# Optimization experiments

Measured on AMD Instinct MI355X. Metric: run time of the kernel, lower is better.

Reference implementation:

```python
import jax, jax.numpy as jnp
import numpy as np

D, H, WIN, OUT = 3, 64, 8, 32
B, T = 128, 129
IU, JU = np.triu_indices(D, k=1)  # Lyndon pairs i<j at depth 2


def setup_inputs() -> dict:
    key = jax.random.key(0)
    ks = jax.random.split(key, 10)
    ts = jnp.broadcast_to(jnp.linspace(0.0, 1.0, T), (B, T))
    # path-like control values: cumulative sum of small increments
    x = jnp.cumsum(0.1 * jax.random.normal(ks[0], (B, T, D)), axis=1)
    def lin(k, o, i):
        return jax.random.normal(k, (o, i), dtype=jnp.float32) * (1.0 / np.sqrt(i))
    return {
        "ts": ts, "x": x,
        "W0": lin(ks[1], 128, D), "b0": jnp.zeros((128,), jnp.float32),
        "W1": lin(ks[2], 128, 128), "b1": jnp.zeros((128,), jnp.float32),
        "W2": lin(ks[3], H, 128), "b2": jnp.zeros((H,), jnp.float32),
        "V0": lin(ks[4], 128, H), "c0": jnp.zeros((128,), jnp.float32),
        "V1": lin(ks[5], 128, 128), "c1": jnp.zeros((128,), jnp.float32),
        "V2": lin(ks[6], D * H, 128), "c2": jnp.zeros((D * H,), jnp.float32),
        "R": lin(ks[7], OUT, H), "rb": jnp.zeros((OUT,), jnp.float32),
    }


def reference(ts, x, W0, b0, W1, b1, W2, b2, V0, c0, V1, c1, V2, c2, R, rb):
    sp = jax.nn.softplus

    def init_mlp(v):  # R^D -> R^H, Euclidean retract = identity
        return W2 @ sp(W1 @ sp(W0 @ v + b0) + b1) + b2

    def vf_flat(y):  # R^H -> R^{D*H}, final tanh (split_multi_vector_field)
        return jnp.tanh(V2 @ sp(V1 @ sp(V0 @ y + c0) + c1) + c2)

    def F(y):
        # level-1 fields f_i(y) as rows of m: (D, H)
        m = vf_flat(y).reshape(D, H)
        # J[a, b] = D f_b(y) . f_a(y)  via JVPs in directions f_a
        J = jax.vmap(lambda v: jax.jvp(vf_flat, (y,), (v,))[1].reshape(D, H))(m)
        # Lyndon level-2 brackets [f_i, f_j] = Df_j.f_i - Df_i.f_j
        br = J[IU, JU] - J[JU, IU]  # (D*(D-1)/2, H)
        return jnp.concatenate([m, br], axis=0).T  # (H, logsig_size)

    def logsigs_fn(xs):  # depth-2 log-signatures over disjoint windows
        nw = (T - 1) // WIN
        idx = (np.arange(nw) * WIN)[:, None] + np.arange(WIN + 1)[None, :]
        win = xs[idx]
        lvl1 = win[:, -1] - win[:, 0]       # increments
        rel = win[:, :-1] - win[:, :1]      # path relative to window start
        dv = win[:, 1:] - win[:, :-1]       # increments within window
        a = jnp.einsum('nki,nkj->nij', rel, dv)
        area = 0.5 * (a - jnp.swapaxes(a, 1, 2))  # Levy areas
        return jnp.concatenate([lvl1, area[:, IU, JU]], axis=1)

    def solve_one(t, xs):
        h0 = init_mlp(xs[0])
        ls = logsigs_fn(xs)                       # (nw, L)
        t_sig = t[::WIN]                          # window knot times
        slopes = ls / (t_sig[1:] - t_sig[:-1])[:, None]  # dz/dt per window
        slope_steps = jnp.repeat(slopes, WIN, axis=0)    # (T-1, L)
        dts = t[1:] - t[:-1]

        def step(y, inp):  # Heun integration of dy = F(y) dz/dt dt
            dt, s = inp
            k1 = F(y) @ s
            k2 = F(y + dt * k1) @ s
            yn = y + 0.5 * dt * (k1 + k2)
            return yn, yn

        _, ys = jax.lax.scan(step, h0, (dts, slope_steps))
        hidden = jnp.concatenate([h0[None], ys], axis=0)  # (T, H)
        return jnp.tanh(hidden @ R.T + rb)                # evolving readout

    return jax.vmap(solve_one)(ts, x)  # (B, T, OUT)
```

## Files before the change

### kernel.cpp

```cpp
#include <hip/hip_runtime.h>
#include <math.h>

#define BB 128
#define TT 129
#define NSTEP 128
#define NW 16
#define WINW 8
#define OUTD 32

typedef _Float16 h2_t __attribute__((ext_vector_type(2)));

__device__ __forceinline__ float fast_rcp(float v){ return __builtin_amdgcn_rcpf(v); }
__device__ __forceinline__ float softplus_f(float v){ return fmaxf(v,0.f)+__logf(1.f+__expf(-fabsf(v))); }
__device__ __forceinline__ float sigmoid_f(float v){ return fast_rcp(1.f+__expf(-v)); }
__device__ __forceinline__ float tanh_f(float v){
    float ax=fminf(fabsf(v),15.f); float e=__expf(2.f*ax);
    float r=1.f-2.f*fast_rcp(e+1.f); return copysignf(r,v);
}
__device__ __forceinline__ float pack2(float a,float b){
    h2_t h; h.x=(_Float16)a; h.y=(_Float16)b; return __builtin_bit_cast(float,h);
}
__device__ __forceinline__ float dot2c(float wc,float ac,float acc){
    return __builtin_amdgcn_fdot2(__builtin_bit_cast(h2_t,wc),__builtin_bit_cast(h2_t,ac),acc,false);
}
__device__ __forceinline__ float dot2q(float4 wq,float4 aq,float acc){
    acc=dot2c(wq.x,aq.x,acc); acc=dot2c(wq.y,aq.y,acc);
    acc=dot2c(wq.z,aq.z,acc); acc=dot2c(wq.w,aq.w,acc); return acc;
}
#define DOT4(acc,Wv,Av) acc += (Wv).x*(Av).x + (Wv).y*(Av).y + (Wv).z*(Av).z + (Wv).w*(Av).w
#define PIN4(v) asm volatile("" : "+v"((v).x), "+v"((v).y), "+v"((v).z), "+v"((v).w))

#define DPPF(x,ctrl) __builtin_bit_cast(float, __builtin_amdgcn_update_dpp(0, __builtin_bit_cast(int,(x)), (ctrl), 0xF, 0xF, true))
__device__ __forceinline__ float dpp_xor1(float x){ return DPPF(x,0xB1); }
__device__ __forceinline__ float dpp_xor2(float x){ return DPPF(x,0x4E); }
__device__ __forceinline__ float dpp_hmir(float x){ return DPPF(x,0x141); }
#define RED8(x) do{ x += dpp_xor1(x); x += dpp_xor2(x); x += dpp_hmir(x); }while(0)

__global__ __launch_bounds__(512, 1)
void ncde_solve(const float* __restrict__ ts, const float* __restrict__ x,
                const float* __restrict__ W0, const float* __restrict__ b0,
                const float* __restrict__ W1, const float* __restrict__ b1,
                const float* __restrict__ W2, const float* __restrict__ b2,
                const float* __restrict__ V0, const float* __restrict__ c0,
                const float* __restrict__ V1, const float* __restrict__ c1,
                const float* __restrict__ V2, const float* __restrict__ c2,
                const float* __restrict__ R, const float* __restrict__ rb,
                float* __restrict__ out)
{
    const int b = blockIdx.x;
    const int t = threadIdx.x;
    const int r = t >> 3, q = t & 7;
    const int prow = t >> 3, poct = t & 7;

    __shared__ __align__(16) float RSh[OUTD*68];
    __shared__ __align__(16) float ySh[64];
    __shared__ __align__(16) float yp[32], y2p[32];
    __shared__ __align__(16) float a0H[64], a1H[64];
    __shared__ __align__(16) float mpH[96];
    __shared__ __align__(16) float u0H[192], u1H[192];
    __shared__ float slopesSh[NW][6];
    __shared__ float dtsSh[NSTEP];

    float4 v0c[2], v1c[2][2], v2c[3][2];
    {
        auto pkld = [](const float* src)->float4{
            const float4* p=(const float4*)src;
            float4 a=p[0], c=p[1];
            float4 rr; rr.x=pack2(a.x,a.y); rr.y=pack2(a.z,a.w); rr.z=pack2(c.x,c.y); rr.w=pack2(c.z,c.w);
            return rr;
        };
        #pragma unroll
        for (int i=0;i<2;i++) v0c[i]=pkld(V0 + (r+64*i)*64 + q*8);
        #pragma unroll
        for (int i=0;i<2;i++){
            const float* base = V1 + (r+64*i)*128 + q*16;
            v1c[i][0]=pkld(base); v1c[i][1]=pkld(base+8);
        }
        #pragma unroll
        for (int i=0;i<3;i++){
            const float* base = V2 + (r+64*i)*128 + q*16;
            v2c[i][0]=pkld(base); v2c[i][1]=pkld(base+8);
        }
        #pragma unroll
        for (int i=0;i<2;i++) PIN4(v0c[i]);
        #pragma unroll
        for (int i=0;i<2;i++){ PIN4(v1c[i][0]); PIN4(v1c[i][1]); }
        #pragma unroll
        for (int i=0;i<3;i++){ PIN4(v2c[i][0]); PIN4(v2c[i][1]); }
    }
    const float c0A=c0[r], c0B=c0[64+r];
    const float c1A=c1[r], c1B=c1[64+r];
    const float c2A=c2[r], c2B=c2[64+r], c2C=c2[128+r];
    const float rbp = rb[prow & 31];

    for (int i=t; i<OUTD*64; i+=512) RSh[(i>>6)*68 + (i&63)] = R[i];
    const float* tsb = ts + (size_t)b*TT;
    if (t < NSTEP) dtsSh[t] = tsb[t+1] - tsb[t];

    if (t < NW) {
        const int w = t;
        const float* xs = x + (size_t)(b*TT + w*WINW)*3;
        float x0c[3] = {xs[0], xs[1], xs[2]};
        float prev[3] = {x0c[0], x0c[1], x0c[2]};
        float am01=0.f, am02=0.f, am12=0.f, am10=0.f, am20=0.f, am21=0.f;
        #pragma unroll
        for (int k=0;k<WINW;k++) {
            float cur[3] = {xs[(k+1)*3+0], xs[(k+1)*3+1], xs[(k+1)*3+2]};
            float rel[3], dv[3];
            #pragma unroll
            for (int c=0;c<3;c++){ rel[c]=prev[c]-x0c[c]; dv[c]=cur[c]-prev[c]; }
            am01 += rel[0]*dv[1]; am10 += rel[1]*dv[0];
            am02 += rel[0]*dv[2]; am20 += rel[2]*dv[0];
            am12 += rel[1]*dv[2]; am21 += rel[2]*dv[1];
            prev[0]=cur[0]; prev[1]=cur[1]; prev[2]=cur[2];
        }
        const float invden = 1.f/(tsb[(w+1)*WINW] - tsb[w*WINW]);
        slopesSh[w][0] = (prev[0]-x0c[0])*invden;
        slopesSh[w][1] = (prev[1]-x0c[1])*invden;
        slopesSh[w][2] = (prev[2]-x0c[2])*invden;
        slopesSh[w][3] = 0.5f*(am01-am10)*invden;
        slopesSh[w][4] = 0.5f*(am02-am20)*invden;
        slopesSh[w][5] = 0.5f*(am12-am21)*invden;
    }

    if (t < 128) {
        const float xv0 = x[(size_t)b*TT*3+0];
        const float xv1 = x[(size_t)b*TT*3+1];
        const float xv2 = x[(size_t)b*TT*3+2];
        float acc = b0[t] + W0[t*3]*xv0 + W0[t*3+1]*xv1 + W0[t*3+2]*xv2;
        u0H[t] = softplus_f(acc);
    }
    __syncthreads();
    if (t < 128) {
        float acc = b1[t];
        const float4* rw = (const float4*)(W1 + t*128);
        #pragma unroll 8
        for (int k=0;k<32;k++){ float4 wv=rw[k]; float4 av=*(const float4*)&u0H[4*k]; DOT4(acc,wv,av); }
        u1H[t] = softplus_f(acc);
    }
    __syncthreads();
    if (t < 64) {
        float acc = b2[t];
        const float4* rw = (const float4*)(W2 + t*128);
        #pragma unroll 8
        for (int k=0;k<32;k++){ float4 wv=rw[k]; float4 av=*(const float4*)&u1H[4*k]; DOT4(acc,wv,av); }
        ySh[t] = acc;
        ((_Float16*)yp)[t] = (_Float16)acc;
    }
    __syncthreads();

    float yreg = ySh[r];
    float k1r = 0.f;
    float S0,S1,S2,S3,S4,S5;

    auto Feval = [&](const float* ypIn, bool first, float dtc) {
        float sig0A,sig0B,sig1A,sig1B,mA,mB,mC,dtA,dtB,dtC;
        {
            float4 y0 = ((const float4*)ypIn)[q];
            float zA=dot2q(v0c[0],y0,0.f);
            float zB=dot2q(v0c[1],y0,0.f);
            RED8(zA); RED8(zB);
            zA += c0A; zB += c0B;
            sig0A=sigmoid_f(zA); sig0B=sigmoid_f(zB);
            if (!q){
                ((_Float16*)a0H)[r]    = (_Float16)softplus_f(zA);
                ((_Float16*)a0H)[64+r] = (_Float16)softplus_f(zB);
            }
        }
        __syncthreads();
        {
            const float4* A = (const float4*)a0H + q*2;
            float4 a0=A[0], a1=A[1];
            float zA=dot2q(v1c[0][0],a0,0.f); zA=dot2q(v1c[0][1],a1,zA);
            float zB=dot2q(v1c[1][0],a0,0.f); zB=dot2q(v1c[1][1],a1,zB);
            RED8(zA); RED8(zB);
            zA += c1A; zB += c1B;
            sig1A=sigmoid_f(zA); sig1B=sigmoid_f(zB);
            if (!q){
                ((_Float16*)a1H)[r]    = (_Float16)softplus_f(zA);
                ((_Float16*)a1H)[64+r] = (_Float16)softplus_f(zB);
            }
        }
        __syncthreads();
        {
            const float4* A = (const float4*)a1H + q*2;
            float4 a0=A[0], a1=A[1];
            float zA=dot2q(v2c[0][0],a0,0.f); zA=dot2q(v2c[0][1],a1,zA);
            float zB=dot2q(v2c[1][0],a0,0.f); zB=dot2q(v2c[1][1],a1,zB);
            float zC=dot2q(v2c[2][0],a0,0.f); zC=dot2q(v2c[2][1],a1,zC);
            RED8(zA); RED8(zB); RED8(zC);
            mA=tanh_f(zA+c2A); mB=tanh_f(zB+c2B); mC=tanh_f(zC+c2C);
            dtA=1.f-mA*mA; dtB=1.f-mB*mB; dtC=1.f-mC*mC;
            if (!q){
                ((_Float16*)mpH)[r]     = (_Float16)mA;
                ((_Float16*)mpH)[64+r]  = (_Float16)mB;
                ((_Float16*)mpH)[128+r] = (_Float16)mC;
            }
        }
        __syncthreads();
        {
            const float4* M = (const float4*)mpH;
            float4 g0=M[q], g1=M[8+q], g2=M[16+q];
            float t0A=dot2q(v0c[0],g0,0.f), t1A=dot2q(v0c[0],g1,0.f), t2A=dot2q(v0c[0],g2,0.f);
            float t0B=dot2q(v0c[1],g0,0.f), t1B=dot2q(v0c[1],g1,0.f), t2B=dot2q(v0c[1],g2,0.f);
            RED8(t0A); RED8(t1A); RED8(t2A);
            RED8(t0B); RED8(t1B); RED8(t2B);
            if (!q){
                ((_Float16*)u0H)[r]      = (_Float16)(sig0A*t0A);
                ((_Float16*)u0H)[64+r]   = (_Float16)(sig0B*t0B);
                ((_Float16*)u0H)[128+r]  = (_Float16)(sig0A*t1A);
                ((_Float16*)u0H)[192+r]  = (_Float16)(sig0B*t1B);
                ((_Float16*)u0H)[256+r]  = (_Float16)(sig0A*t2A);
                ((_Float16*)u0H)[320+r]  = (_Float16)(sig0B*t2B);
            }
        }
        __syncthreads();
        {
            const float4* U = (const float4*)u0H;
            float4 g0a=U[q*2],    g0b=U[q*2+1];
            float4 g1a=U[16+q*2], g1b=U[16+q*2+1];
            float4 g2a=U[32+q*2], g2b=U[32+q*2+1];
            float t0A=dot2q(v1c[0][0],g0a,0.f); t0A=dot2q(v1c[0][1],g0b,t0A);
            float t1A=dot2q(v1c[0][0],g1a,0.f); t1A=dot2q(v1c[0][1],g1b,t1A);
            float t2A=dot2q(v1c[0][0],g2a,0.f); t2A=dot2q(v1c[0][1],g2b,t2A);
            float t0B=dot2q(v1c[1][0],g0a,0.f); t0B=dot2q(v1c[1][1],g0b,t0B);
            float t1B=dot2q(v1c[1][0],g1a,0.f); t1B=dot2q(v1c[1][1],g1b,t1B);
            float t2B=dot2q(v1c[1][0],g2a,0.f); t2B=dot2q(v1c[1][1],g2b,t2B);
            RED8(t0A); RED8(t1A); RED8(t2A);
            RED8(t0B); RED8(t1B); RED8(t2B);
            if (!q){
                ((_Float16*)u1H)[r]      = (_Float16)(sig1A*t0A);
                ((_Float16*)u1H)[64+r]   = (_Float16)(sig1B*t0B);
                ((_Float16*)u1H)[128+r]  = (_Float16)(sig1A*t1A);
                ((_Float16*)u1H)[192+r]  = (_Float16)(sig1B*t1B);
                ((_Float16*)u1H)[256+r]  = (_Float16)(sig1A*t2A);
                ((_Float16*)u1H)[320+r]  = (_Float16)(sig1B*t2B);
            }
        }
        __syncthreads();
        {
            const float4* U = (const float4*)u1H;
            float4 g0a=U[q*2],    g0b=U[q*2+1];
            float4 g1a=U[16+q*2], g1b=U[16+q*2+1];
            float4 g2a=U[32+q*2], g2b=U[32+q*2+1];
            float J1r=dot2q(v2c[0][0],g1a,0.f); J1r=dot2q(v2c[0][1],g1b,J1r);
            float J2r=dot2q(v2c[0][0],g2a,0.f); J2r=dot2q(v2c[0][1],g2b,J2r);
            float J0m=dot2q(v2c[1][0],g0a,0.f); J0m=dot2q(v2c[1][1],g0b,J0m);
            float J2m=dot2q(v2c[1][0],g2a,0.f); J2m=dot2q(v2c[1][1],g2b,J2m);
            float J0t=dot2q(v2c[2][0],g0a,0.f); J0t=dot2q(v2c[2][1],g0b,J0t);
            float J1t=dot2q(v2c[2][0],g1a,0.f); J1t=dot2q(v2c[2][1],g1b,J1t);
            RED8(J1r); RED8(J2r); RED8(J0m); RED8(J2m); RED8(J0t); RED8(J1t);
            J1r*=dtA; J2r*=dtA; J0m*=dtB; J2m*=dtB; J0t*=dtC; J1t*=dtC;
            float kk = mA*S0 + mB*S1 + mC*S2
                     + S3*(J0m - J1r) + S4*(J0t - J2r) + S5*(J1t - J2m);
            if (first){
                k1r = kk;
                float y2 = yreg + dtc*kk;
                if (!q) ((_Float16*)y2p)[r] = (_Float16)y2;
            } else {
                yreg += 0.5f*dtc*(k1r + kk);
                if (!q){ ((_Float16*)yp)[r] = (_Float16)yreg; ySh[r] = yreg; }
            }
        }
        __syncthreads();
    };

    auto proj = [&](int stp) {
        if (t < 256){
            const float4* rr = (const float4*)(RSh + prow*68 + poct*8);
            const float4* yy = (const float4*)(ySh + poct*8);
            float pacc = 0.f;
            DOT4(pacc, rr[0], yy[0]); DOT4(pacc, rr[1], yy[1]);
            pacc += dpp_xor1(pacc);
            pacc += dpp_xor2(pacc);
            pacc += dpp_hmir(pacc);
            if (!poct) out[(size_t)(b*TT + stp)*OUTD + prow] = tanh_f(pacc + rbp);
        }
    };

    for (int step=0; step<NSTEP; ++step) {
        proj(step);
        const int w = step >> 3;
        S0=slopesSh[w][0]; S1=slopesSh[w][1]; S2=slopesSh[w][2];
        S3=slopesSh[w][3]; S4=slopesSh[w][4]; S5=slopesSh[w][5];
        const float dtc = dtsSh[step];
        Feval(yp,  true,  dtc);
        Feval(y2p, false, dtc);
    }
    proj(NSTEP);
}

extern "C" void kernel_launch(void* const* d_in, const int* in_sizes, int n_in,
                              void* d_out, int out_size, void* d_ws, size_t ws_size,
                              hipStream_t stream) {
    const float* ts = (const float*)d_in[0];
    const float* x  = (const float*)d_in[1];
    const float* W0 = (const float*)d_in[2];
    const float* b0 = (const float*)d_in[3];
    const float* W1 = (const float*)d_in[4];
    const float* b1 = (const float*)d_in[5];
    const float* W2 = (const float*)d_in[6];
    const float* b2 = (const float*)d_in[7];
    const float* V0 = (const float*)d_in[8];
    const float* c0 = (const float*)d_in[9];
    const float* V1 = (const float*)d_in[10];
    const float* c1 = (const float*)d_in[11];
    const float* V2 = (const float*)d_in[12];
    const float* c2 = (const float*)d_in[13];
    const float* R  = (const float*)d_in[14];
    const float* rb = (const float*)d_in[15];
    float* out = (float*)d_out;

    ncde_solve<<<dim3(BB), dim3(512), 0, stream>>>(
        ts, x, W0, b0, W1, b1, W2, b2, V0, c0, V1, c1, V2, c2, R, rb, out);
}
```

Before: 692.0 us.

## Remap threads to four lanes per row and fuse sigmoid/softplus exp

Changes the thread mapping from 8 lanes per output row covering 64 rows to 4 lanes per row covering 128 rows. Each thread now owns a single layer row instead of two, and the dot-product reductions shrink from three DPP steps to two. The three final-layer outputs are split across the two halves of the block, and the projection moves to the upper half. A combined sigmoid/softplus helper shares one exp and one reciprocal per activation. The upper half now stays idle during the last Jacobian stage, and per-thread register weight storage grows.

```diff
diff --git a/kernel.cpp b/kernel.cpp
--- a/kernel.cpp
+++ b/kernel.cpp
@@ -11,11 +11,15 @@
 typedef _Float16 h2_t __attribute__((ext_vector_type(2)));
 
 __device__ __forceinline__ float fast_rcp(float v){ return __builtin_amdgcn_rcpf(v); }
-__device__ __forceinline__ float softplus_f(float v){ return fmaxf(v,0.f)+__logf(1.f+__expf(-fabsf(v))); }
-__device__ __forceinline__ float sigmoid_f(float v){ return fast_rcp(1.f+__expf(-v)); }
 __device__ __forceinline__ float tanh_f(float v){
     float ax=fminf(fabsf(v),15.f); float e=__expf(2.f*ax);
     float r=1.f-2.f*fast_rcp(e+1.f); return copysignf(r,v);
+}
+__device__ __forceinline__ void sigsp(float z, float& sp, float& sig){
+    float e  = __expf(-fabsf(z));
+    float rc = fast_rcp(1.f+e);
+    sp  = fmaxf(z,0.f) + __logf(1.f+e);
+    sig = (z>=0.f) ? rc : e*rc;
 }
 __device__ __forceinline__ float pack2(float a,float b){
     h2_t h; h.x=(_Float16)a; h.y=(_Float16)b; return __builtin_bit_cast(float,h);
@@ -34,7 +38,7 @@
 __device__ __forceinline__ float dpp_xor1(float x){ return DPPF(x,0xB1); }
 __device__ __forceinline__ float dpp_xor2(float x){ return DPPF(x,0x4E); }
 __device__ __forceinline__ float dpp_hmir(float x){ return DPPF(x,0x141); }
-#define RED8(x) do{ x += dpp_xor1(x); x += dpp_xor2(x); x += dpp_hmir(x); }while(0)
+#define RED4(x) do{ x += dpp_xor1(x); x += dpp_xor2(x); }while(0)
 
 __global__ __launch_bounds__(512, 1)
 void ncde_solve(const float* __restrict__ ts, const float* __restrict__ x,
@@ -49,8 +53,10 @@
 {
     const int b = blockIdx.x;
     const int t = threadIdx.x;
-    const int r = t >> 3, q = t & 7;
-    const int prow = t >> 3, poct = t & 7;
+    const int r = t >> 2, q = t & 3;
+    const int rl = r & 63;
+    const int pt = (t >= 256) ? (t - 256) : 0;
+    const int prow = pt >> 3, poct = pt & 7;
 
     __shared__ __align__(16) float RSh[OUTD*68];
     __shared__ __align__(16) float ySh[64];
@@ -58,10 +64,11 @@
     __shared__ __align__(16) float a0H[64], a1H[64];
     __shared__ __align__(16) float mpH[96];
     __shared__ __align__(16) float u0H[192], u1H[192];
+    __shared__ float mF32[64];
     __shared__ float slopesSh[NW][6];
     __shared__ float dtsSh[NSTEP];
 
-    float4 v0c[2], v1c[2][2], v2c[3][2];
+    float4 v0c[2], v1c[4], v2c[3][4];
     {
         auto pkld = [](const float* src)->float4{
             const float4* p=(const float4*)src;
@@ -69,28 +76,32 @@
             float4 rr; rr.x=pack2(a.x,a.y); rr.y=pack2(a.z,a.w); rr.z=pack2(c.x,c.y); rr.w=pack2(c.z,c.w);
             return rr;
         };
-        #pragma unroll
-        for (int i=0;i<2;i++) v0c[i]=pkld(V0 + (r+64*i)*64 + q*8);
-        #pragma unroll
-        for (int i=0;i<2;i++){
-            const float* base = V1 + (r+64*i)*128 + q*16;
-            v1c[i][0]=pkld(base); v1c[i][1]=pkld(base+8);
+        {
+            const float* base = V0 + r*64 + q*16;
+            v0c[0]=pkld(base); v0c[1]=pkld(base+8);
+        }
+        {
+            const float* base = V1 + r*128 + q*32;
+            #pragma unroll
+            for (int k=0;k<4;k++) v1c[k]=pkld(base+8*k);
         }
         #pragma unroll
         for (int i=0;i<3;i++){
-            const float* base = V2 + (r+64*i)*128 + q*16;
-            v2c[i][0]=pkld(base); v2c[i][1]=pkld(base+8);
-        }
+            const float* base = V2 + (rl+64*i)*128 + q*32;
+            #pragma unroll
+            for (int k=0;k<4;k++) v2c[i][k]=pkld(base+8*k);
+        }
+        PIN4(v0c[0]); PIN4(v0c[1]);
         #pragma unroll
-        for (int i=0;i<2;i++) PIN4(v0c[i]);
+        for (int k=0;k<4;k++) PIN4(v1c[k]);
         #pragma unroll
-        for (int i=0;i<2;i++){ PIN4(v1c[i][0]); PIN4(v1c[i][1]); }
-        #pragma unroll
-        for (int i=0;i<3;i++){ PIN4(v2c[i][0]); PIN4(v2c[i][1]); }
-    }
-    const float c0A=c0[r], c0B=c0[64+r];
-    const float c1A=c1[r], c1B=c1[64+r];
-    const float c2A=c2[r], c2B=c2[64+r], c2C=c2[128+r];
+        for (int i=0;i<3;i++){
+            #pragma unroll
+            for (int k=0;k<4;k++) PIN4(v2c[i][k]);
+        }
+    }
+    const float c0r=c0[r], c1r=c1[r];
+    const float c2a=c2[rl], c2b=c2[64+rl], c2c=c2[128+rl];
     const float rbp = rb[prow & 31];
 
     for (int i=t; i<OUTD*64; i+=512) RSh[(i>>6)*68 + (i&63)] = R[i];
@@ -128,7 +139,8 @@
         const float xv1 = x[(size_t)b*TT*3+1];
         const float xv2 = x[(size_t)b*TT*3+2];
         float acc = b0[t] + W0[t*3]*xv0 + W0[t*3+1]*xv1 + W0[t*3+2]*xv2;
-        u0H[t] = softplus_f(acc);
+        float sp, sg; sigsp(acc, sp, sg);
+        u0H[t] = sp;
     }
     __syncthreads();
     if (t < 128) {
@@ -136,7 +148,8 @@
         const float4* rw = (const float4*)(W1 + t*128);
         #pragma unroll 8
         for (int k=0;k<32;k++){ float4 wv=rw[k]; float4 av=*(const float4*)&u0H[4*k]; DOT4(acc,wv,av); }
-        u1H[t] = softplus_f(acc);
+        float sp, sg; sigsp(acc, sp, sg);
+        u1H[t] = sp;
     }
     __syncthreads();
     if (t < 64) {
@@ -149,124 +162,119 @@
     }
     __syncthreads();
 
-    float yreg = ySh[r];
+    float yreg = (r < 64) ? ySh[r] : 0.f;
     float k1r = 0.f;
     float S0,S1,S2,S3,S4,S5;
 
     auto Feval = [&](const float* ypIn, bool first, float dtc) {
-        float sig0A,sig0B,sig1A,sig1B,mA,mB,mC,dtA,dtB,dtC;
-        {
-            float4 y0 = ((const float4*)ypIn)[q];
-            float zA=dot2q(v0c[0],y0,0.f);
-            float zB=dot2q(v0c[1],y0,0.f);
-            RED8(zA); RED8(zB);
-            zA += c0A; zB += c0B;
-            sig0A=sigmoid_f(zA); sig0B=sigmoid_f(zB);
+        float sig0r, sig1r, mA=0.f, mC=0.f;
+        {
+            const float4* Y = (const float4*)ypIn;
+            float z = dot2q(v0c[0], Y[q*2], 0.f);
+            z = dot2q(v0c[1], Y[q*2+1], z);
+            RED4(z); z += c0r;
+            float sp; sigsp(z, sp, sig0r);
+            if (!q) ((_Float16*)a0H)[r] = (_Float16)sp;
+        }
+        __syncthreads();
+        {
+            const float4* A = (const float4*)a0H + q*4;
+            float z = 0.f;
+            #pragma unroll
+            for (int k=0;k<4;k++) z = dot2q(v1c[k], A[k], z);
+            RED4(z); z += c1r;
+            float sp; sigsp(z, sp, sig1r);
+            if (!q) ((_Float16*)a1H)[r] = (_Float16)sp;
+        }
+        __syncthreads();
+        {
+            const float4* A = (const float4*)a1H + q*4;
+            float4 a0=A[0],a1=A[1],a2=A[2],a3=A[3];
+            if (r < 64){
+                float zA=dot2q(v2c[0][0],a0,0.f); zA=dot2q(v2c[0][1],a1,zA); zA=dot2q(v2c[0][2],a2,zA); zA=dot2q(v2c[0][3],a3,zA);
+                float zC=dot2q(v2c[2][0],a0,0.f); zC=dot2q(v2c[2][1],a1,zC); zC=dot2q(v2c[2][2],a2,zC); zC=dot2q(v2c[2][3],a3,zC);
+                RED4(zA); RED4(zC);
+                mA = tanh_f(zA + c2a); mC = tanh_f(zC + c2c);
+                if (!q){
+                    ((_Float16*)mpH)[rl]     = (_Float16)mA;
+                    ((_Float16*)mpH)[128+rl] = (_Float16)mC;
+                }
+            } else {
+                float zB=dot2q(v2c[1][0],a0,0.f); zB=dot2q(v2c[1][1],a1,zB); zB=dot2q(v2c[1][2],a2,zB); zB=dot2q(v2c[1][3],a3,zB);
+                RED4(zB);
+                float mB = tanh_f(zB + c2b);
+                if (!q){
+                    ((_Float16*)mpH)[64+rl] = (_Float16)mB;
+                    mF32[rl] = mB;
+                }
+            }
+        }
+        __syncthreads();
+        {
+            const float4* M = (const float4*)mpH;
+            float4 g0a=M[q*2],    g0b=M[q*2+1];
+            float4 g1a=M[8+q*2],  g1b=M[8+q*2+1];
+            float4 g2a=M[16+q*2], g2b=M[16+q*2+1];
+            float t0=dot2q(v0c[0],g0a,0.f); t0=dot2q(v0c[1],g0b,t0);
+            float t1=dot2q(v0c[0],g1a,0.f); t1=dot2q(v0c[1],g1b,t1);
+            float t2=dot2q(v0c[0],g2a,0.f); t2=dot2q(v0c[1],g2b,t2);
+            RED4(t0); RED4(t1); RED4(t2);
             if (!q){
-                ((_Float16*)a0H)[r]    = (_Float16)softplus_f(zA);
-                ((_Float16*)a0H)[64+r] = (_Float16)softplus_f(zB);
-            }
-        }
-        __syncthreads();
-        {
-            const float4* A = (const float4*)a0H + q*2;
-            float4 a0=A[0], a1=A[1];
-            float zA=dot2q(v1c[0][0],a0,0.f); zA=dot2q(v1c[0][1],a1,zA);
-            float zB=dot2q(v1c[1][0],a0,0.f); zB=dot2q(v1c[1][1],a1,zB);
-            RED8(zA); RED8(zB);
-            zA += c1A; zB += c1B;
-            sig1A=sigmoid_f(zA); sig1B=sigmoid_f(zB);
+                ((_Float16*)u0H)[r]     = (_Float16)(sig0r*t0);
+                ((_Float16*)u0H)[128+r] = (_Float16)(sig0r*t1);
+                ((_Float16*)u0H)[256+r] = (_Float16)(sig0r*t2);
+            }
+        }
+        __syncthreads();
+        {
+            const float4* U = (const float4*)u0H;
+            float t0=0.f,t1=0.f,t2=0.f;
+            #pragma unroll
+            for (int k=0;k<4;k++){
+                float4 w = v1c[k];
+                t0=dot2q(w,U[q*4+k],t0); t1=dot2q(w,U[16+q*4+k],t1); t2=dot2q(w,U[32+q*4+k],t2);
+            }
+            RED4(t0); RED4(t1); RED4(t2);
             if (!q){
-                ((_Float16*)a1H)[r]    = (_Float16)softplus_f(zA);
-                ((_Float16*)a1H)[64+r] = (_Float16)softplus_f(zB);
-            }
-        }
-        __syncthreads();
-        {
-            const float4* A = (const float4*)a1H + q*2;
-            float4 a0=A[0], a1=A[1];
-            float zA=dot2q(v2c[0][0],a0,0.f); zA=dot2q(v2c[0][1],a1,zA);
-            float zB=dot2q(v2c[1][0],a0,0.f); zB=dot2q(v2c[1][1],a1,zB);
-            float zC=dot2q(v2c[2][0],a0,0.f); zC=dot2q(v2c[2][1],a1,zC);
-            RED8(zA); RED8(zB); RED8(zC);
-            mA=tanh_f(zA+c2A); mB=tanh_f(zB+c2B); mC=tanh_f(zC+c2C);
-            dtA=1.f-mA*mA; dtB=1.f-mB*mB; dtC=1.f-mC*mC;
-            if (!q){
-                ((_Float16*)mpH)[r]     = (_Float16)mA;
-                ((_Float16*)mpH)[64+r]  = (_Float16)mB;
-                ((_Float16*)mpH)[128+r] = (_Float16)mC;
-            }
-        }
-        __syncthreads();
-        {
-            const float4* M = (const float4*)mpH;
-            float4 g0=M[q], g1=M[8+q], g2=M[16+q];
-            float t0A=dot2q(v0c[0],g0,0.f), t1A=dot2q(v0c[0],g1,0.f), t2A=dot2q(v0c[0],g2,0.f);
-            float t0B=dot2q(v0c[1],g0,0.f), t1B=dot2q(v0c[1],g1,0.f), t2B=dot2q(v0c[1],g2,0.f);
-            RED8(t0A); RED8(t1A); RED8(t2A);
-            RED8(t0B); RED8(t1B); RED8(t2B);
-            if (!q){
-                ((_Float16*)u0H)[r]      = (_Float16)(sig0A*t0A);
-                ((_Float16*)u0H)[64+r]   = (_Float16)(sig0B*t0B);
-                ((_Float16*)u0H)[128+r]  = (_Float16)(sig0A*t1A);
-                ((_Float16*)u0H)[192+r]  = (_Float16)(sig0B*t1B);
-                ((_Float16*)u0H)[256+r]  = (_Float16)(sig0A*t2A);
-                ((_Float16*)u0H)[320+r]  = (_Float16)(sig0B*t2B);
-            }
-        }
-        __syncthreads();
-        {
-            const float4* U = (const float4*)u0H;
-            float4 g0a=U[q*2],    g0b=U[q*2+1];
-            float4 g1a=U[16+q*2], g1b=U[16+q*2+1];
-            float4 g2a=U[32+q*2], g2b=U[32+q*2+1];
-            float t0A=dot2q(v1c[0][0],g0a,0.f); t0A=dot2q(v1c[0][1],g0b,t0A);
-            float t1A=dot2q(v1c[0][0],g1a,0.f); t1A=dot2q(v1c[0][1],g1b,t1A);
-            float t2A=dot2q(v1c[0][0],g2a,0.f); t2A=dot2q(v1c[0][1],g2b,t2A);
-            float t0B=dot2q(v1c[1][0],g0a,0.f); t0B=dot2q(v1c[1][1],g0b,t0B);
-            float t1B=dot2q(v1c[1][0],g1a,0.f); t1B=dot2q(v1c[1][1],g1b,t1B);
-            float t2B=dot2q(v1c[1][0],g2a,0.f); t2B=dot2q(v1c[1][1],g2b,t2B);
-            RED8(t0A); RED8(t1A); RED8(t2A);
-            RED8(t0B); RED8(t1B); RED8(t2B);
-            if (!q){
-                ((_Float16*)u1H)[r]      = (_Float16)(sig1A*t0A);
-                ((_Float16*)u1H)[64+r]   = (_Float16)(sig1B*t0B);
-                ((_Float16*)u1H)[128+r]  = (_Float16)(sig1A*t1A);
-                ((_Float16*)u1H)[192+r]  = (_Float16)(sig1B*t1B);
-                ((_Float16*)u1H)[256+r]  = (_Float16)(sig1A*t2A);
-                ((_Float16*)u1H)[320+r]  = (_Float16)(sig1B*t2B);
-            }
-        }
-        __syncthreads();
-        {
+                ((_Float16*)u1H)[r]     = (_Float16)(sig1r*t0);
+                ((_Float16*)u1H)[128+r] = (_Float16)(sig1r*t1);
+                ((_Float16*)u1H)[256+r] = (_Float16)(sig1r*t2);
+            }
+        }
+        __syncthreads();
+        if (r < 64){
             const float4* U = (const float4*)u1H;
-            float4 g0a=U[q*2],    g0b=U[q*2+1];
-            float4 g1a=U[16+q*2], g1b=U[16+q*2+1];
-            float4 g2a=U[32+q*2], g2b=U[32+q*2+1];
-            float J1r=dot2q(v2c[0][0],g1a,0.f); J1r=dot2q(v2c[0][1],g1b,J1r);
-            float J2r=dot2q(v2c[0][0],g2a,0.f); J2r=dot2q(v2c[0][1],g2b,J2r);
-            float J0m=dot2q(v2c[1][0],g0a,0.f); J0m=dot2q(v2c[1][1],g0b,J0m);
-            float J2m=dot2q(v2c[1][0],g2a,0.f); J2m=dot2q(v2c[1][1],g2b,J2m);
-            float J0t=dot2q(v2c[2][0],g0a,0.f); J0t=dot2q(v2c[2][1],g0b,J0t);
-            float J1t=dot2q(v2c[2][0],g1a,0.f); J1t=dot2q(v2c[2][1],g1b,J1t);
-            RED8(J1r); RED8(J2r); RED8(J0m); RED8(J2m); RED8(J0t); RED8(J1t);
+            float4 g0[4],g1[4],g2[4];
+            #pragma unroll
+            for (int k=0;k<4;k++){ g0[k]=U[q*4+k]; g1[k]=U[16+q*4+k]; g2[k]=U[32+q*4+k]; }
+            float J1r=0.f,J2r=0.f,J0m=0.f,J2m=0.f,J0t=0.f,J1t=0.f;
+            #pragma unroll
+            for (int k=0;k<4;k++){
+                float4 wa=v2c[0][k], wb=v2c[1][k], wc=v2c[2][k];
+                J1r=dot2q(wa,g1[k],J1r); J2r=dot2q(wa,g2[k],J2r);
+                J0m=dot2q(wb,g0[k],J0m); J2m=dot2q(wb,g2[k],J2m);
+                J0t=dot2q(wc,g0[k],J0t); J1t=dot2q(wc,g1[k],J1t);
+            }
+            RED4(J1r); RED4(J2r); RED4(J0m); RED4(J2m); RED4(J0t); RED4(J1t);
+            const float mB = mF32[rl];
+            const float dtA = 1.f-mA*mA, dtB = 1.f-mB*mB, dtC = 1.f-mC*mC;
             J1r*=dtA; J2r*=dtA; J0m*=dtB; J2m*=dtB; J0t*=dtC; J1t*=dtC;
             float kk = mA*S0 + mB*S1 + mC*S2
                      + S3*(J0m - J1r) + S4*(J0t - J2r) + S5*(J1t - J2m);
             if (first){
                 k1r = kk;
                 float y2 = yreg + dtc*kk;
-                if (!q) ((_Float16*)y2p)[r] = (_Float16)y2;
+                if (!q) ((_Float16*)y2p)[rl] = (_Float16)y2;
             } else {
                 yreg += 0.5f*dtc*(k1r + kk);
-                if (!q){ ((_Float16*)yp)[r] = (_Float16)yreg; ySh[r] = yreg; }
+                if (!q){ ((_Float16*)yp)[rl] = (_Float16)yreg; ySh[rl] = yreg; }
             }
         }
         __syncthreads();
     };
 
     auto proj = [&](int stp) {
-        if (t < 256){
+        if (t >= 256){
             const float4* rr = (const float4*)(RSh + prow*68 + poct*8);
             const float4* yy = (const float4*)(ySh + poct*8);
             float pacc = 0.f;
```

After: 596.9 us. -13.7%, faster.
